# Kernel tuning notes

Measured on AMD Instinct MI355X. Metric: run time of the kernel, lower is better.

## Reference

```python
import jax, jax.numpy as jnp
import numpy as np

B, T, C, H = 4, 4096, 1024, 64


def setup_inputs() -> dict:
    key = jax.random.key(0)
    ks = jax.random.split(key, 7)
    s = C ** -0.5
    return {
        "x": jax.random.normal(ks[0], (B, T, C), dtype=jnp.float32),
        "Wk": jax.random.normal(ks[1], (C, H), dtype=jnp.float32) * s,
        "bk": jax.random.normal(ks[2], (H,), dtype=jnp.float32) * 0.02,
        "Wq": jax.random.normal(ks[3], (C, H), dtype=jnp.float32) * s,
        "bq": jax.random.normal(ks[4], (H,), dtype=jnp.float32) * 0.02,
        "Wv": jax.random.normal(ks[5], (C, H), dtype=jnp.float32) * s,
        "bv": jax.random.normal(ks[6], (H,), dtype=jnp.float32) * 0.02,
    }


def reference(x, Wk, bk, Wq, bq, Wv, bv):
    Bx, Tx, Cx = x.shape
    k = x @ Wk + bk            # [B,T,H]
    q = x @ Wq + bq            # [B,T,H]
    v = x @ Wv + bv            # [B,T,H]
    scale = Cx ** -0.5         # NOTE: source scales by n_embed^-0.5, not head_size
    # Faithful to source: scores = K @ Q^T (rows indexed by key position)
    wei = jnp.einsum("bth,bsh->bts", k, q) * scale  # [B,T,T]
    causal = jnp.tril(jnp.ones((Tx, Tx), dtype=bool))
    wei = jnp.where(causal, wei, -jnp.inf)
    wei = jax.nn.softmax(wei, axis=-1)
    out = jnp.einsum("bts,bsh->bth", wei, v)        # [B,T,H]
    return out
```

## Files before the change

### kernel.cpp

```cpp
#include <hip/hip_runtime.h>
#include <hip/hip_bf16.h>
#include <math.h>


typedef __attribute__((ext_vector_type(8))) short bf16x8;
typedef __attribute__((ext_vector_type(4))) short bf16x4;
typedef __attribute__((ext_vector_type(4))) float f32x4;

#define MFMA16(a, b, c) __builtin_amdgcn_mfma_f32_16x16x32_bf16(a, b, c, 0, 0, 0)

__device__ __forceinline__ short f2bf(float f) {
    union { float f; unsigned u; } v; v.f = f;
    unsigned r = v.u + 0x7FFFu + ((v.u >> 16) & 1u);
    return (short)(r >> 16);
}

static constexpr int T = 4096;
static constexpr int C = 1024;
static constexpr int H = 64;
static constexpr int BATCH = 4;
static constexpr int M = BATCH * T;
static constexpr int CPB = 288;
static constexpr float LOG2E = 1.44269504088896340736f;
static constexpr float KSCALE = 0.03125f * LOG2E;

__global__ __launch_bounds__(256) void wtrans_kernel(
    const float* __restrict__ Wk, const float* __restrict__ Wq,
    const float* __restrict__ Wv, short* __restrict__ Wt_g)
{
    const int blk = blockIdx.x;
    const int tid = threadIdx.x;
    __shared__ short Wl[64][72];
    const int mat = blk / 16, k0 = (blk % 16) * 64;
    const float* W = (mat == 0) ? Wk : (mat == 1) ? Wq : Wv;
    const int hr = (tid & 15) * 4, kr = tid >> 4;
    #pragma unroll
    for (int pass = 0; pass < 4; ++pass) {
        int k = kr + pass * 16;
        float4 v = *(const float4*)&W[(size_t)(k0 + k) * H + hr];
        Wl[hr + 0][k] = f2bf(v.x);
        Wl[hr + 1][k] = f2bf(v.y);
        Wl[hr + 2][k] = f2bf(v.z);
        Wl[hr + 3][k] = f2bf(v.w);
    }
    __syncthreads();
    const int h = tid >> 2, kk = (tid & 3) * 16;
    bf16x8 o0 = *(const bf16x8*)&Wl[h][kk];
    bf16x8 o1 = *(const bf16x8*)&Wl[h][kk + 8];
    *(bf16x8*)&Wt_g[(size_t)(mat * 64 + h) * C + k0 + kk] = o0;
    *(bf16x8*)&Wt_g[(size_t)(mat * 64 + h) * C + k0 + kk + 8] = o1;
}

__global__ __launch_bounds__(512) void proj_kernel(
    const float* __restrict__ x, const short* __restrict__ Wt_g,
    const float* __restrict__ bk, const float* __restrict__ bq,
    const float* __restrict__ bv,
    short* __restrict__ Kb, short* __restrict__ Qb, short* __restrict__ Vt)
{
    __shared__ short As[2][64][72];
    __shared__ short Ws[2][192][72];
    const int tid = threadIdx.x;
    const int wv = tid >> 6, lane = tid & 63, quad = lane >> 4, l16 = lane & 15;
    const int grp = wv >> 2, w4 = wv & 3;
    const int m0 = blockIdx.x * 64;
    const int arow = tid >> 3, ac8 = (tid & 7) * 8;

    f32x4 acc[6];
    #pragma unroll
    for (int i = 0; i < 6; ++i)
        for (int j = 0; j < 4; ++j) acc[i][j] = 0.f;

    float4 xa0, xa1;
    bf16x8 wl[3];
    auto gload = [&](int k0) {
        xa0 = *(const float4*)&x[(size_t)(m0 + arow) * C + k0 + ac8];
        xa1 = *(const float4*)&x[(size_t)(m0 + arow) * C + k0 + ac8 + 4];
        #pragma unroll
        for (int i = 0; i < 3; ++i) {
            int idx = tid + i * 512;
            wl[i] = *(const bf16x8*)&Wt_g[(size_t)(idx >> 3) * C + k0 + (idx & 7) * 8];
        }
    };
    auto lwrite = [&](int p) {
        bf16x8 av;
        av[0] = f2bf(xa0.x); av[1] = f2bf(xa0.y); av[2] = f2bf(xa0.z); av[3] = f2bf(xa0.w);
        av[4] = f2bf(xa1.x); av[5] = f2bf(xa1.y); av[6] = f2bf(xa1.z); av[7] = f2bf(xa1.w);
        *(bf16x8*)&As[p][arow][ac8] = av;
        #pragma unroll
        for (int i = 0; i < 3; ++i) {
            int idx = tid + i * 512;
            *(bf16x8*)&Ws[p][idx >> 3][(idx & 7) * 8] = wl[i];
        }
    };

    gload(0);
    lwrite(0);
    __syncthreads();
    for (int it = 0; it < 16; ++it) {
        const int p = it & 1;
        if (it < 15) gload((it + 1) * 64);
        bf16x8 a0 = *(const bf16x8*)&As[p][w4 * 16 + l16][quad * 8];
        bf16x8 a1 = *(const bf16x8*)&As[p][w4 * 16 + l16][32 + quad * 8];
        #pragma unroll
        for (int tn = 0; tn < 6; ++tn) {
            bf16x8 b0 = *(const bf16x8*)&Ws[p][grp * 96 + tn * 16 + l16][quad * 8];
            bf16x8 b1 = *(const bf16x8*)&Ws[p][grp * 96 + tn * 16 + l16][32 + quad * 8];
            acc[tn] = MFMA16(a0, b0, acc[tn]);
            acc[tn] = MFMA16(a1, b1, acc[tn]);
        }
        if (it < 15) {
            lwrite((it + 1) & 1);
            __syncthreads();
        }
    }
    #pragma unroll
    for (int tn = 0; tn < 6; ++tn) {
        int gc = grp * 96 + tn * 16 + l16;
        int mat = gc >> 6, h = gc & 63;
        const float* bias = (mat == 0) ? bk : (mat == 1) ? bq : bv;
        float bb = bias[h];
        float sc = (mat == 0) ? KSCALE : 1.f;
        #pragma unroll
        for (int r = 0; r < 4; ++r) {
            int row = m0 + w4 * 16 + quad * 4 + r;
            short val = f2bf((acc[tn][r] + bb) * sc);
            if (mat == 0)      Kb[(size_t)row * H + h] = val;
            else if (mat == 1) Qb[(size_t)row * H + h] = val;
            else               Vt[((size_t)(row >> 6)) * 4096 + h * 64 + (row & 63)] = val;
        }
    }
}

__device__ __forceinline__ void chunk_map8(int c, int& tt, int& chunk) {
    int k = 1;
    while (c >= 4 * k * (k + 1)) ++k;
    int off = c - 4 * k * (k - 1);
    int q = off / k;
    tt = 8 * (k - 1) + q;
    chunk = off - q * k;
}

__global__ __launch_bounds__(256) void attn_part_kernel(
    const short* __restrict__ Kb, const short* __restrict__ Qb,
    const short* __restrict__ Vt, float* __restrict__ Pb,
    float* __restrict__ lnPb)
{
    __shared__ short Pl[4][2][16][76];
    __shared__ float Ob[64][66];
    __shared__ float lnb[64];
    const int tid = threadIdx.x;
    const int wv = tid >> 6, lane = tid & 63;
    const int quad = lane >> 4, l16 = lane & 15;
    const int sp = wv & 1, sh = wv >> 1;
    const int g = blockIdx.x;
    const int b = g & 3;
    const int c = CPB - 1 - (g >> 2);
    int tt, chunk;
    chunk_map8(c, tt, chunk);
    const int t0 = tt * 64;
    const int sA = sp * 2, sB = sp * 2 + 1;
    const int st0 = chunk * 8;
    const int st1 = min(st0 + 8, tt + 1);
    const size_t base = (size_t)b * T * H;

    const short* krA = Kb + base + (size_t)(t0 + sA * 16 + l16) * H;
    const short* krB = Kb + base + (size_t)(t0 + sB * 16 + l16) * H;
    bf16x8 kf0a = *(const bf16x8*)(krA + quad * 8);
    bf16x8 kf1a = *(const bf16x8*)(krA + 32 + quad * 8);
    bf16x8 kf0b = *(const bf16x8*)(krB + quad * 8);
    bf16x8 kf1b = *(const bf16x8*)(krB + 32 + quad * 8);

    bf16x8 ones;
    #pragma unroll
    for (int j = 0; j < 8; ++j) ones[j] = (short)0x3F80;

    f32x4 oA[4], oB[4], lnA, lnB;
    #pragma unroll
    for (int i = 0; i < 4; ++i)
        for (int j = 0; j < 4; ++j) { oA[i][j] = 0.f; oB[i][j] = 0.f; }
    #pragma unroll
    for (int j = 0; j < 4; ++j) { lnA[j] = 0.f; lnB[j] = 0.f; }

    const int myb = st0 + sh;
    const short* qp = Qb + base + (size_t)(myb * 64 + l16) * H + quad * 8;
    const short* vp = Vt + ((size_t)(b * 64 + myb)) * 4096 + l16 * 64 + quad * 8;

    bf16x8 qc0[4], qc1[4];
    if (myb < st1) {
        #pragma unroll
        for (int tn = 0; tn < 4; ++tn) {
            qc0[tn] = *(const bf16x8*)(qp + tn * 1024);
            qc1[tn] = *(const bf16x8*)(qp + tn * 1024 + 32);
        }
    }

    for (int st = myb; st < st1; st += 2) {
        bf16x8 vb0[4], vb1[4];
        #pragma unroll
        for (int hn = 0; hn < 4; ++hn) {
            vb0[hn] = *(const bf16x8*)(vp + hn * 1024);
            vb1[hn] = *(const bf16x8*)(vp + hn * 1024 + 32);
        }
        f32x4 sAc[4], sBc[4];
        #pragma unroll
        for (int tn = 0; tn < 4; ++tn) {
            #pragma unroll
            for (int j = 0; j < 4; ++j) { sAc[tn][j] = 0.f; sBc[tn][j] = 0.f; }
            sAc[tn] = MFMA16(qc0[tn], kf0a, sAc[tn]);
            sAc[tn] = MFMA16(qc1[tn], kf1a, sAc[tn]);
            sBc[tn] = MFMA16(qc0[tn], kf0b, sBc[tn]);
            sBc[tn] = MFMA16(qc1[tn], kf1b, sBc[tn]);
        }
        const size_t qoff = (st + 2 < st1) ? 8192 : 0;
        #pragma unroll
        for (int tn = 0; tn < 4; ++tn) {
            qc0[tn] = *(const bf16x8*)(qp + qoff + tn * 1024);
            qc1[tn] = *(const bf16x8*)(qp + qoff + tn * 1024 + 32);
        }
        const bool diag = (st == tt);
        #pragma unroll
        for (int tn = 0; tn < 4; ++tn) {
            bf16x4 pa, pb;
            #pragma unroll
            for (int r = 0; r < 4; ++r) {
                float va = sAc[tn][r], vb = sBc[tn][r];
                if (diag) {
                    int scol = tn * 16 + quad * 4 + r;
                    if (scol > sA * 16 + l16) va = -INFINITY;
                    if (scol > sB * 16 + l16) vb = -INFINITY;
                }
                pa[r] = f2bf(exp2f(va));
                pb[r] = f2bf(exp2f(vb));
            }
            *(bf16x4*)&Pl[wv][0][l16][tn * 16 + quad * 4] = pa;
            *(bf16x4*)&Pl[wv][1][l16][tn * 16 + quad * 4] = pb;
        }
        bf16x8 aA0 = *(const bf16x8*)&Pl[wv][0][l16][quad * 8];
        bf16x8 aA1 = *(const bf16x8*)&Pl[wv][0][l16][32 + quad * 8];
        bf16x8 aB0 = *(const bf16x8*)&Pl[wv][1][l16][quad * 8];
        bf16x8 aB1 = *(const bf16x8*)&Pl[wv][1][l16][32 + quad * 8];
        #pragma unroll
        for (int hn = 0; hn < 4; ++hn) {
            oA[hn] = MFMA16(aA0, vb0[hn], oA[hn]);
            oA[hn] = MFMA16(aA1, vb1[hn], oA[hn]);
            oB[hn] = MFMA16(aB0, vb0[hn], oB[hn]);
            oB[hn] = MFMA16(aB1, vb1[hn], oB[hn]);
        }
        lnA = MFMA16(aA0, ones, lnA);
        lnA = MFMA16(aA1, ones, lnA);
        lnB = MFMA16(aB0, ones, lnB);
        lnB = MFMA16(aB1, ones, lnB);
        qp += 8192;
        vp += 8192;
    }

    const int rbase = sp * 32;
    if (sh == 1) {
        #pragma unroll
        for (int hn = 0; hn < 4; ++hn)
            #pragma unroll
            for (int r = 0; r < 4; ++r) {
                Ob[rbase + quad * 4 + r][hn * 16 + l16] = oA[hn][r];
                Ob[rbase + 16 + quad * 4 + r][hn * 16 + l16] = oB[hn][r];
            }
        if (l16 == 0) {
            #pragma unroll
            for (int r = 0; r < 4; ++r) {
                lnb[rbase + quad * 4 + r] = lnA[r];
                lnb[rbase + 16 + quad * 4 + r] = lnB[r];
            }
        }
    }
    __syncthreads();
    if (sh == 0) {
        float* Pc = Pb + (size_t)(b * CPB + c) * 4096;
        #pragma unroll
        for (int hn = 0; hn < 4; ++hn)
            #pragma unroll
            for (int r = 0; r < 4; ++r) {
                int ra = rbase + quad * 4 + r;
                int rb = ra + 16;
                float va = oA[hn][r] + Ob[ra][hn * 16 + l16];
                float vb = oB[hn][r] + Ob[rb][hn * 16 + l16];
                Pc[(size_t)ra * 64 + hn * 16 + l16] = va;
                Pc[(size_t)rb * 64 + hn * 16 + l16] = vb;
            }
        if (l16 == 0) {
            float* lc = lnPb + (size_t)(b * CPB + c) * 64;
            #pragma unroll
            for (int r = 0; r < 4; ++r) {
                lc[rbase + quad * 4 + r] = lnA[r] + lnb[rbase + quad * 4 + r];
                lc[rbase + 16 + quad * 4 + r] = lnB[r] + lnb[rbase + 16 + quad * 4 + r];
            }
        }
    }
}

__global__ __launch_bounds__(256) void reduce_norm_kernel(
    const float* __restrict__ Pb, const float* __restrict__ lnPb,
    float* __restrict__ out)
{
    const int blk = blockIdx.x;
    const int b = blk >> 6, tt = blk & 63;
    const int k = tt / 8 + 1;
    const int base_c = 4 * k * (k - 1) + (tt - 8 * (k - 1)) * k;
    const int tid = threadIdx.x;
    __shared__ float lnS[64];
    if (tid < 64) {
        float s = 0.f;
        for (int i = 0; i < k; ++i)
            s += lnPb[(size_t)(b * CPB + base_c + i) * 64 + tid];
        lnS[tid] = 1.f / s;
    }
    __syncthreads();
    float4 acc[4];
    #pragma unroll
    for (int j = 0; j < 4; ++j) acc[j] = {0.f, 0.f, 0.f, 0.f};
    for (int i = 0; i < k; ++i) {
        const float4* p4 = (const float4*)(Pb + (size_t)(b * CPB + base_c + i) * 4096);
        #pragma unroll
        for (int j = 0; j < 4; ++j) {
            float4 v = p4[tid + j * 256];
            acc[j].x += v.x; acc[j].y += v.y; acc[j].z += v.z; acc[j].w += v.w;
        }
    }
    float4* o4 = (float4*)out;
    const size_t obase = ((size_t)b * T + tt * 64) * 16;
    #pragma unroll
    for (int j = 0; j < 4; ++j) {
        int idx = tid + j * 256;
        float inv = lnS[idx >> 4];
        float4 v = acc[j];
        v.x *= inv; v.y *= inv; v.z *= inv; v.w *= inv;
        o4[obase + idx] = v;
    }
}

extern "C" void kernel_launch(void* const* d_in, const int* in_sizes, int n_in,
                              void* d_out, int out_size, void* d_ws, size_t ws_size,
                              hipStream_t stream) {
    const float* x  = (const float*)d_in[0];
    const float* Wk = (const float*)d_in[1];
    const float* bk = (const float*)d_in[2];
    const float* Wq = (const float*)d_in[3];
    const float* bq = (const float*)d_in[4];
    const float* Wv = (const float*)d_in[5];
    const float* bv = (const float*)d_in[6];
    float* out = (float*)d_out;

    char* ws = (char*)d_ws;
    size_t off = 0;
    short* Kb   = (short*)(ws + off); off += (size_t)M * H * 2;
    short* Qb   = (short*)(ws + off); off += (size_t)M * H * 2;
    short* Vt   = (short*)(ws + off); off += (size_t)M * H * 2;
    short* Wt_g = (short*)(ws + off); off += (size_t)192 * C * 2;
    float* Pb   = (float*)(ws + off); off += (size_t)BATCH * CPB * 4096 * 4;
    float* lnPb = (float*)(ws + off); off += (size_t)BATCH * CPB * 64 * 4;

    wtrans_kernel<<<48, 256, 0, stream>>>(Wk, Wq, Wv, Wt_g);
    proj_kernel<<<M / 64, 512, 0, stream>>>(x, Wt_g, bk, bq, bv, Kb, Qb, Vt);
    attn_part_kernel<<<BATCH * CPB, 256, 0, stream>>>(Kb, Qb, Vt, Pb, lnPb);
    reduce_norm_kernel<<<BATCH * 64, 256, 0, stream>>>(Pb, lnPb, out);
}
```

Before: 179.7 us.

## Fold weight transpose into projection and fuse reduction into attention via atomic counters

Removes the separate weight-transpose kernel: the projection kernel now reads fp32 Wk/Wq/Wv directly and transposes them into padded shared memory while converting. The separate reduce/normalize kernel is also removed. Single-chunk tiles write normalized output directly, and multi-chunk tiles use a per-tile atomic counter so the last finishing block performs the reduction. This cuts two launches and the Wt_g round trip, at the cost of redundant per-block weight conversion, scalar strided LDS writes, and threadfence/atomic overhead.

```diff
diff --git a/kernel.cpp b/kernel.cpp
--- a/kernel.cpp
+++ b/kernel.cpp
@@ -24,46 +24,25 @@
 static constexpr float LOG2E = 1.44269504088896340736f;
 static constexpr float KSCALE = 0.03125f * LOG2E;
 
-__global__ __launch_bounds__(256) void wtrans_kernel(
+__global__ __launch_bounds__(512) void proj_kernel(
+    const float* __restrict__ x,
     const float* __restrict__ Wk, const float* __restrict__ Wq,
-    const float* __restrict__ Wv, short* __restrict__ Wt_g)
-{
-    const int blk = blockIdx.x;
-    const int tid = threadIdx.x;
-    __shared__ short Wl[64][72];
-    const int mat = blk / 16, k0 = (blk % 16) * 64;
-    const float* W = (mat == 0) ? Wk : (mat == 1) ? Wq : Wv;
-    const int hr = (tid & 15) * 4, kr = tid >> 4;
-    #pragma unroll
-    for (int pass = 0; pass < 4; ++pass) {
-        int k = kr + pass * 16;
-        float4 v = *(const float4*)&W[(size_t)(k0 + k) * H + hr];
-        Wl[hr + 0][k] = f2bf(v.x);
-        Wl[hr + 1][k] = f2bf(v.y);
-        Wl[hr + 2][k] = f2bf(v.z);
-        Wl[hr + 3][k] = f2bf(v.w);
-    }
-    __syncthreads();
-    const int h = tid >> 2, kk = (tid & 3) * 16;
-    bf16x8 o0 = *(const bf16x8*)&Wl[h][kk];
-    bf16x8 o1 = *(const bf16x8*)&Wl[h][kk + 8];
-    *(bf16x8*)&Wt_g[(size_t)(mat * 64 + h) * C + k0 + kk] = o0;
-    *(bf16x8*)&Wt_g[(size_t)(mat * 64 + h) * C + k0 + kk + 8] = o1;
-}
-
-__global__ __launch_bounds__(512) void proj_kernel(
-    const float* __restrict__ x, const short* __restrict__ Wt_g,
+    const float* __restrict__ Wv,
     const float* __restrict__ bk, const float* __restrict__ bq,
     const float* __restrict__ bv,
-    short* __restrict__ Kb, short* __restrict__ Qb, short* __restrict__ Vt)
+    short* __restrict__ Kb, short* __restrict__ Qb, short* __restrict__ Vt,
+    int* __restrict__ cnt)
 {
     __shared__ short As[2][64][72];
-    __shared__ short Ws[2][192][72];
+    __shared__ short Ws[2][192][74];
     const int tid = threadIdx.x;
     const int wv = tid >> 6, lane = tid & 63, quad = lane >> 4, l16 = lane & 15;
     const int grp = wv >> 2, w4 = wv & 3;
     const int m0 = blockIdx.x * 64;
     const int arow = tid >> 3, ac8 = (tid & 7) * 8;
+    const int kr = tid >> 3, h8 = (tid & 7) * 8;
+
+    if (blockIdx.x == 0 && tid < BATCH * 64) cnt[tid] = 0;
 
     f32x4 acc[6];
     #pragma unroll
@@ -71,26 +50,32 @@
         for (int j = 0; j < 4; ++j) acc[i][j] = 0.f;
 
     float4 xa0, xa1;
-    bf16x8 wl[3];
+    float4 wk0, wk1, wq0, wq1, wv0, wv1;
     auto gload = [&](int k0) {
         xa0 = *(const float4*)&x[(size_t)(m0 + arow) * C + k0 + ac8];
         xa1 = *(const float4*)&x[(size_t)(m0 + arow) * C + k0 + ac8 + 4];
-        #pragma unroll
-        for (int i = 0; i < 3; ++i) {
-            int idx = tid + i * 512;
-            wl[i] = *(const bf16x8*)&Wt_g[(size_t)(idx >> 3) * C + k0 + (idx & 7) * 8];
-        }
+        const size_t wo = (size_t)(k0 + kr) * H + h8;
+        wk0 = *(const float4*)&Wk[wo];  wk1 = *(const float4*)&Wk[wo + 4];
+        wq0 = *(const float4*)&Wq[wo];  wq1 = *(const float4*)&Wq[wo + 4];
+        wv0 = *(const float4*)&Wv[wo];  wv1 = *(const float4*)&Wv[wo + 4];
     };
     auto lwrite = [&](int p) {
         bf16x8 av;
         av[0] = f2bf(xa0.x); av[1] = f2bf(xa0.y); av[2] = f2bf(xa0.z); av[3] = f2bf(xa0.w);
         av[4] = f2bf(xa1.x); av[5] = f2bf(xa1.y); av[6] = f2bf(xa1.z); av[7] = f2bf(xa1.w);
         *(bf16x8*)&As[p][arow][ac8] = av;
-        #pragma unroll
-        for (int i = 0; i < 3; ++i) {
-            int idx = tid + i * 512;
-            *(bf16x8*)&Ws[p][idx >> 3][(idx & 7) * 8] = wl[i];
-        }
+        Ws[p][h8 + 0][kr] = f2bf(wk0.x);  Ws[p][h8 + 1][kr] = f2bf(wk0.y);
+        Ws[p][h8 + 2][kr] = f2bf(wk0.z);  Ws[p][h8 + 3][kr] = f2bf(wk0.w);
+        Ws[p][h8 + 4][kr] = f2bf(wk1.x);  Ws[p][h8 + 5][kr] = f2bf(wk1.y);
+        Ws[p][h8 + 6][kr] = f2bf(wk1.z);  Ws[p][h8 + 7][kr] = f2bf(wk1.w);
+        Ws[p][64 + h8 + 0][kr] = f2bf(wq0.x);  Ws[p][64 + h8 + 1][kr] = f2bf(wq0.y);
+        Ws[p][64 + h8 + 2][kr] = f2bf(wq0.z);  Ws[p][64 + h8 + 3][kr] = f2bf(wq0.w);
+        Ws[p][64 + h8 + 4][kr] = f2bf(wq1.x);  Ws[p][64 + h8 + 5][kr] = f2bf(wq1.y);
+        Ws[p][64 + h8 + 6][kr] = f2bf(wq1.z);  Ws[p][64 + h8 + 7][kr] = f2bf(wq1.w);
+        Ws[p][128 + h8 + 0][kr] = f2bf(wv0.x); Ws[p][128 + h8 + 1][kr] = f2bf(wv0.y);
+        Ws[p][128 + h8 + 2][kr] = f2bf(wv0.z); Ws[p][128 + h8 + 3][kr] = f2bf(wv0.w);
+        Ws[p][128 + h8 + 4][kr] = f2bf(wv1.x); Ws[p][128 + h8 + 5][kr] = f2bf(wv1.y);
+        Ws[p][128 + h8 + 6][kr] = f2bf(wv1.z); Ws[p][128 + h8 + 7][kr] = f2bf(wv1.w);
     };
 
     gload(0);
@@ -143,11 +128,14 @@
 __global__ __launch_bounds__(256) void attn_part_kernel(
     const short* __restrict__ Kb, const short* __restrict__ Qb,
     const short* __restrict__ Vt, float* __restrict__ Pb,
-    float* __restrict__ lnPb)
+    float* __restrict__ lnPb, float* __restrict__ out,
+    int* __restrict__ cnt)
 {
     __shared__ short Pl[4][2][16][76];
     __shared__ float Ob[64][66];
     __shared__ float lnb[64];
+    __shared__ float lnS[64];
+    __shared__ int lastFlag;
     const int tid = threadIdx.x;
     const int wv = tid >> 6, lane = tid & 63;
     const int quad = lane >> 4, l16 = lane & 15;
@@ -272,6 +260,31 @@
         }
     }
     __syncthreads();
+
+    const int k = tt / 8 + 1;
+    if (k == 1) {
+        if (sh == 0) {
+            float invA[4], invB[4];
+            #pragma unroll
+            for (int r = 0; r < 4; ++r) {
+                invA[r] = 1.f / (lnA[r] + lnb[rbase + quad * 4 + r]);
+                invB[r] = 1.f / (lnB[r] + lnb[rbase + 16 + quad * 4 + r]);
+            }
+            #pragma unroll
+            for (int hn = 0; hn < 4; ++hn)
+                #pragma unroll
+                for (int r = 0; r < 4; ++r) {
+                    int ra = rbase + quad * 4 + r;
+                    int rb = ra + 16;
+                    float va = (oA[hn][r] + Ob[ra][hn * 16 + l16]) * invA[r];
+                    float vb = (oB[hn][r] + Ob[rb][hn * 16 + l16]) * invB[r];
+                    out[base + (size_t)(t0 + ra) * H + hn * 16 + l16] = va;
+                    out[base + (size_t)(t0 + rb) * H + hn * 16 + l16] = vb;
+                }
+        }
+        return;
+    }
+
     if (sh == 0) {
         float* Pc = Pb + (size_t)(b * CPB + c) * 4096;
         #pragma unroll
@@ -294,18 +307,15 @@
             }
         }
     }
-}
-
-__global__ __launch_bounds__(256) void reduce_norm_kernel(
-    const float* __restrict__ Pb, const float* __restrict__ lnPb,
-    float* __restrict__ out)
-{
-    const int blk = blockIdx.x;
-    const int b = blk >> 6, tt = blk & 63;
-    const int k = tt / 8 + 1;
+    __threadfence();
+    __syncthreads();
+    if (tid == 0)
+        lastFlag = (atomicAdd(&cnt[b * 64 + tt], 1) == k - 1);
+    __syncthreads();
+    if (!lastFlag) return;
+
+    __threadfence();
     const int base_c = 4 * k * (k - 1) + (tt - 8 * (k - 1)) * k;
-    const int tid = threadIdx.x;
-    __shared__ float lnS[64];
     if (tid < 64) {
         float s = 0.f;
         for (int i = 0; i < k; ++i)
@@ -313,24 +323,24 @@
         lnS[tid] = 1.f / s;
     }
     __syncthreads();
-    float4 acc[4];
-    #pragma unroll
-    for (int j = 0; j < 4; ++j) acc[j] = {0.f, 0.f, 0.f, 0.f};
+    float4 racc[4];
+    #pragma unroll
+    for (int j = 0; j < 4; ++j) racc[j] = {0.f, 0.f, 0.f, 0.f};
     for (int i = 0; i < k; ++i) {
         const float4* p4 = (const float4*)(Pb + (size_t)(b * CPB + base_c + i) * 4096);
         #pragma unroll
         for (int j = 0; j < 4; ++j) {
             float4 v = p4[tid + j * 256];
-            acc[j].x += v.x; acc[j].y += v.y; acc[j].z += v.z; acc[j].w += v.w;
+            racc[j].x += v.x; racc[j].y += v.y; racc[j].z += v.z; racc[j].w += v.w;
         }
     }
     float4* o4 = (float4*)out;
-    const size_t obase = ((size_t)b * T + tt * 64) * 16;
+    const size_t obase = ((size_t)b * T + (size_t)tt * 64) * 16;
     #pragma unroll
     for (int j = 0; j < 4; ++j) {
         int idx = tid + j * 256;
         float inv = lnS[idx >> 4];
-        float4 v = acc[j];
+        float4 v = racc[j];
         v.x *= inv; v.y *= inv; v.z *= inv; v.w *= inv;
         o4[obase + idx] = v;
     }
@@ -353,12 +363,12 @@
     short* Kb   = (short*)(ws + off); off += (size_t)M * H * 2;
     short* Qb   = (short*)(ws + off); off += (size_t)M * H * 2;
     short* Vt   = (short*)(ws + off); off += (size_t)M * H * 2;
-    short* Wt_g = (short*)(ws + off); off += (size_t)192 * C * 2;
     float* Pb   = (float*)(ws + off); off += (size_t)BATCH * CPB * 4096 * 4;
     float* lnPb = (float*)(ws + off); off += (size_t)BATCH * CPB * 64 * 4;
-
-    wtrans_kernel<<<48, 256, 0, stream>>>(Wk, Wq, Wv, Wt_g);
-    proj_kernel<<<M / 64, 512, 0, stream>>>(x, Wt_g, bk, bq, bv, Kb, Qb, Vt);
-    attn_part_kernel<<<BATCH * CPB, 256, 0, stream>>>(Kb, Qb, Vt, Pb, lnPb);
-    reduce_norm_kernel<<<BATCH * 64, 256, 0, stream>>>(Pb, lnPb, out);
-}
+    int*   cnt  = (int*)(ws + off);   off += (size_t)BATCH * 64 * 4;
+
+    proj_kernel<<<M / 64, 512, 0, stream>>>(x, Wk, Wq, Wv, bk, bq, bv,
+                                            Kb, Qb, Vt, cnt);
+    attn_part_kernel<<<BATCH * CPB, 256, 0, stream>>>(Kb, Qb, Vt, Pb, lnPb,
+                                                      out, cnt);
+}
```

Measured after the change: 311.0 us. 73.0% more time.
